# Kernel tuning notes

Measured on AMD Instinct MI355X. Metric: run time of the kernel, lower is better.

## Reference

```python
import jax, jax.numpy as jnp
import numpy as np

H_DIM = 2048
D_FF = 4 * H_DIM
NUM_EXPERTS = 8
NUM_SHARED = 2
BATCH, SEQ = 2, 2048


def setup_inputs() -> dict:
    key = jax.random.key(0)
    ks = jax.random.split(key, 10)
    s = 0.02
    return {
        "x": jax.random.normal(ks[0], (BATCH, SEQ, H_DIM), dtype=jnp.float32),
        "ws_w1": jax.random.normal(ks[1], (NUM_SHARED, H_DIM, D_FF), dtype=jnp.float32) * s,
        "ws_b1": jnp.zeros((NUM_SHARED, D_FF), dtype=jnp.float32),
        "ws_w2": jax.random.normal(ks[2], (NUM_SHARED, D_FF, H_DIM), dtype=jnp.float32) * s,
        "ws_b2": jnp.zeros((NUM_SHARED, H_DIM), dtype=jnp.float32),
        "we_w1": jax.random.normal(ks[3], (NUM_EXPERTS, H_DIM, D_FF), dtype=jnp.float32) * s,
        "we_b1": jnp.zeros((NUM_EXPERTS, D_FF), dtype=jnp.float32),
        "we_w2": jax.random.normal(ks[4], (NUM_EXPERTS, D_FF, H_DIM), dtype=jnp.float32) * s,
        "we_b2": jnp.zeros((NUM_EXPERTS, H_DIM), dtype=jnp.float32),
        "wg": jax.random.normal(ks[5], (H_DIM, NUM_EXPERTS), dtype=jnp.float32) * s,
        "top_k": 2,
    }


def reference(x, ws_w1, ws_b1, ws_w2, ws_b2, we_w1, we_b1, we_w2, we_b2, wg, top_k):
    B, S, D = x.shape
    xt = x.reshape(-1, D)  # [T, D], T = B*S
    T = xt.shape[0]

    # ---- shared experts: sum over NUM_SHARED dense MLPs ----
    hs = jax.nn.relu(jnp.einsum('td,ndf->ntf', xt, ws_w1) + ws_b1[:, None, :])
    shared = jnp.einsum('ntf,nfd->td', hs, ws_w2) + ws_b2.sum(axis=0)  # [T, D]

    # ---- sparse top-k routed MoE ----
    logits = xt @ wg                       # [T, E] router logits
    probs = jax.nn.softmax(logits, axis=-1)
    topv, topi = jax.lax.top_k(probs, top_k)
    gates = jnp.zeros_like(probs).at[jnp.arange(T)[:, None], topi].set(topv)  # [T, E]

    moe = jnp.zeros_like(xt)
    for e in range(we_w1.shape[0]):  # small fixed expert count
        he = jax.nn.relu(xt @ we_w1[e] + we_b1[e])
        ye = he @ we_w2[e] + we_b2[e]
        moe = moe + gates[:, e:e + 1] * ye

    out = (shared + moe).reshape(B, S, D)
    return out, logits
```

## Files before the change

kernel.cpp:

```cpp
#include <hip/hip_runtime.h>

#define TOKENS 4096
#define HD 2048
#define FF 8192
#define NE 8
#define NS 2

typedef __attribute__((ext_vector_type(8))) short bf16x8;
typedef __attribute__((ext_vector_type(4))) float f32x4;

__device__ __forceinline__ unsigned rnd_bf(unsigned u) {
  return u + 0x7fffu + ((u >> 16) & 1u);
}
__device__ __forceinline__ unsigned short f2bf(float f) {
  unsigned u = __builtin_bit_cast(unsigned, f);
  return (unsigned short)(rnd_bf(u) >> 16);
}

#define GLDS16(gp, lp)                                                         \
  __builtin_amdgcn_global_load_lds(                                            \
      (const __attribute__((address_space(1))) unsigned*)(const void*)(gp),    \
      (__attribute__((address_space(3))) unsigned*)(lp), 16, 0, 0)

__global__ void cast_x_kernel(const float* __restrict__ x, unsigned short* __restrict__ xb) {
  const size_t i = ((size_t)blockIdx.x * 256 + threadIdx.x) * 4;
  float4 v = *(const float4*)(x + i);
  ushort4 o;
  o.x = f2bf(v.x); o.y = f2bf(v.y); o.z = f2bf(v.z); o.w = f2bf(v.w);
  *(ushort4*)(xb + i) = o;
}

__global__ void router_kernel(const float* __restrict__ x, const float* __restrict__ wg,
                              float* __restrict__ logits_out, int* __restrict__ topi,
                              float* __restrict__ topv, int* __restrict__ counts) {
  const int wave = threadIdx.x >> 6, lane = threadIdx.x & 63;
  const int t = blockIdx.x * 4 + wave;
  const float* xr = x + (size_t)t * HD;
  float acc[8];
#pragma unroll
  for (int e = 0; e < 8; ++e) acc[e] = 0.f;
  for (int d = lane; d < HD; d += 64) {
    const float xv = xr[d];
    const float4 w0 = *(const float4*)(wg + (size_t)d * 8);
    const float4 w1 = *(const float4*)(wg + (size_t)d * 8 + 4);
    acc[0] += xv * w0.x; acc[1] += xv * w0.y; acc[2] += xv * w0.z; acc[3] += xv * w0.w;
    acc[4] += xv * w1.x; acc[5] += xv * w1.y; acc[6] += xv * w1.z; acc[7] += xv * w1.w;
  }
#pragma unroll
  for (int e = 0; e < 8; ++e) {
#pragma unroll
    for (int off = 32; off > 0; off >>= 1) acc[e] += __shfl_xor(acc[e], off);
  }
  if (lane == 0) {
    *(float4*)(logits_out + (size_t)t * 8)     = make_float4(acc[0], acc[1], acc[2], acc[3]);
    *(float4*)(logits_out + (size_t)t * 8 + 4) = make_float4(acc[4], acc[5], acc[6], acc[7]);
    float mx = acc[0];
#pragma unroll
    for (int e = 1; e < 8; ++e) mx = fmaxf(mx, acc[e]);
    float p[8], s = 0.f;
#pragma unroll
    for (int e = 0; e < 8; ++e) { p[e] = expf(acc[e] - mx); s += p[e]; }
    const float inv = 1.f / s;
    int i1 = 0;
#pragma unroll
    for (int e = 1; e < 8; ++e) if (acc[e] > acc[i1]) i1 = e;
    int i2 = (i1 == 0) ? 1 : 0;
#pragma unroll
    for (int e = 0; e < 8; ++e) if (e != i1 && acc[e] > acc[i2]) i2 = e;
    topi[2 * t]     = i1; topv[2 * t]     = p[i1] * inv;
    topi[2 * t + 1] = i2; topv[2 * t + 1] = p[i2] * inv;
    atomicAdd(&counts[i1], 1);
    atomicAdd(&counts[i2], 1);
  }
}

__global__ void offs_kernel(const int* __restrict__ counts, int* __restrict__ offs,
                            int* __restrict__ cursors) {
  if (threadIdx.x == 0) {
    int r = 0;
    for (int e = 0; e < NE; ++e) { offs[e] = r; cursors[e] = r; r += counts[e]; }
  }
}

__global__ void gather_kernel(const unsigned short* __restrict__ xb,
                              const int* __restrict__ topi, const float* __restrict__ topv,
                              int* __restrict__ cursors, unsigned short* __restrict__ xg,
                              int* __restrict__ row_token, float* __restrict__ row_gate) {
  const int wave = threadIdx.x >> 6, lane = threadIdx.x & 63;
  const int t = blockIdx.x * 4 + wave;
  const uint4* src = (const uint4*)(xb + (size_t)t * HD);
#pragma unroll
  for (int j = 0; j < 2; ++j) {
    const int e = topi[2 * t + j];
    int pos = 0;
    if (lane == 0) {
      pos = atomicAdd(&cursors[e], 1);
      row_token[pos] = t;
      row_gate[pos] = topv[2 * t + j];
    }
    pos = __shfl(pos, 0);
    uint4* dst = (uint4*)(xg + (size_t)pos * HD);
#pragma unroll
    for (int c = lane; c < 256; c += 64) dst[c] = src[c];
  }
}

template <int K, int N>
__global__ __launch_bounds__(256) void pack_wt(const float* __restrict__ we,
                                               const float* __restrict__ ws,
                                               unsigned short* __restrict__ dstw) {
  const int e = blockIdx.z;
  const float* src = (e < NE) ? (we + (size_t)e * K * N) : (ws + (size_t)(e - NE) * K * N);
  unsigned short* dst = dstw + (size_t)e * K * N;
  const int nt = blockIdx.x * 64;
  const int kt = blockIdx.y * 64;
  __shared__ unsigned short t[64][73];
  const int tid = threadIdx.x;
  const int rr = tid >> 4, cc = (tid & 15) * 4;
#pragma unroll
  for (int i = 0; i < 4; ++i) {
    const int k = rr + i * 16;
    float4 v = *(const float4*)(src + (size_t)(kt + k) * N + nt + cc);
    t[k][cc + 0] = f2bf(v.x);
    t[k][cc + 1] = f2bf(v.y);
    t[k][cc + 2] = f2bf(v.z);
    t[k][cc + 3] = f2bf(v.w);
  }
  __syncthreads();
  const int nr = tid >> 2, kc = (tid & 3) * 16;
  unsigned u[8];
#pragma unroll
  for (int j = 0; j < 8; ++j)
    u[j] = (unsigned)t[kc + 2 * j][nr] | ((unsigned)t[kc + 2 * j + 1][nr] << 16);
  unsigned short* dp = dst + (size_t)(nt + nr) * K + kt + kc;
  uint4 v0; v0.x = u[0]; v0.y = u[1]; v0.z = u[2]; v0.w = u[3];
  uint4 v1; v1.x = u[4]; v1.y = u[5]; v1.z = u[6]; v1.w = u[7];
  *(uint4*)dp = v0;
  *(uint4*)(dp + 8) = v1;
}

template <int MS>
__device__ __forceinline__ void rd_a(bf16x8 (&d)[8], const unsigned short* base,
                                     int wr, int fr, int fq, int swz) {
#pragma unroll
  for (int mi = 0; mi < 4; ++mi)
#pragma unroll
    for (int ks = 0; ks < 2; ++ks)
      d[mi * 2 + ks] = *(const bf16x8*)(base + (wr * 128 + MS * 64 + mi * 16 + fr) * 64 +
                                        (((ks * 4 + fq) ^ swz) << 3));
}
template <int NSUB>
__device__ __forceinline__ void rd_b(bf16x8 (&d)[4], const unsigned short* base,
                                     int wc, int fr, int fq, int swz) {
#pragma unroll
  for (int ni = 0; ni < 2; ++ni)
#pragma unroll
    for (int ks = 0; ks < 2; ++ks)
      d[ni * 2 + ks] = *(const bf16x8*)(base + (wc * 64 + NSUB * 32 + ni * 16 + fr) * 64 +
                                        (((ks * 4 + fq) ^ swz) << 3));
}
template <int MS, int NSUB>
__device__ __forceinline__ void mm16(f32x4 (&acc)[8][4], const bf16x8 (&a)[8],
                                     const bf16x8 (&b)[4]) {
  __builtin_amdgcn_s_setprio(1);
#pragma unroll
  for (int mi = 0; mi < 4; ++mi)
#pragma unroll
    for (int ni = 0; ni < 2; ++ni)
#pragma unroll
      for (int ks = 0; ks < 2; ++ks)
        acc[MS * 4 + mi][NSUB * 2 + ni] = __builtin_amdgcn_mfma_f32_16x16x32_bf16(
            a[mi * 2 + ks], b[ni * 2 + ks], acc[MS * 4 + mi][NSUB * 2 + ni], 0, 0, 0);
  __builtin_amdgcn_s_setprio(0);
}
template <int MS>
__device__ __forceinline__ void mm32(f32x4 (&acc)[8][4], const bf16x8 (&a)[8],
                                     const bf16x8 (&b0)[4], const bf16x8 (&b1)[4]) {
  __builtin_amdgcn_s_setprio(1);
#pragma unroll
  for (int mi = 0; mi < 4; ++mi)
#pragma unroll
    for (int nn = 0; nn < 4; ++nn)
#pragma unroll
      for (int ks = 0; ks < 2; ++ks) {
        const bf16x8& bb = (nn < 2) ? b0[(nn & 1) * 2 + ks] : b1[(nn & 1) * 2 + ks];
        acc[MS * 4 + mi][nn] = __builtin_amdgcn_mfma_f32_16x16x32_bf16(
            a[mi * 2 + ks], bb, acc[MS * 4 + mi][nn], 0, 0, 0);
      }
  __builtin_amdgcn_s_setprio(0);
}

#define PH_BAR_PRE()                                                           \
  __builtin_amdgcn_sched_barrier(0);                                           \
  __builtin_amdgcn_s_barrier();                                                \
  asm volatile("s_waitcnt lgkmcnt(0)" ::: "memory");                           \
  __builtin_amdgcn_sched_barrier(0)
#define PH_BAR_POST()                                                          \
  __builtin_amdgcn_sched_barrier(0);                                           \
  __builtin_amdgcn_s_barrier()

__global__ __launch_bounds__(512, 2) void gemm2p(
    const unsigned short* __restrict__ Ash,
    const unsigned short* __restrict__ Art,
    const unsigned short* __restrict__ wt,
    const float* __restrict__ bE, const float* __restrict__ bS,
    unsigned short* __restrict__ hout,
    const int* __restrict__ counts, const int* __restrict__ offs) {
  constexpr int K = HD;
  constexpr int NBX = FF / 256;
  constexpr int NWG = NBX * 16;
  extern __shared__ unsigned short smem[];

  const int e = blockIdx.z;
  int M;
  const unsigned short* A;
  const float* bias;
  int hbase;
  if (e < NE) {
    M = counts[e];
    A = Art + (size_t)offs[e] * K;
    bias = bE + (size_t)e * FF;
    hbase = offs[e];
  } else {
    M = TOKENS;
    A = Ash;
    bias = bS + (size_t)(e - NE) * FF;
    hbase = 2 * TOKENS + (e - NE) * TOKENS;
  }
  const unsigned short* Bt = wt + (size_t)e * HD * FF;

  int flat = blockIdx.x + NBX * blockIdx.y;
  flat = (flat & 7) * (NWG >> 3) + (flat >> 3);
  const int m0 = (flat & 15) * 256;
  const int n0 = (flat >> 4) * 256;
  if (m0 >= M) return;

  const int tid = threadIdx.x;
  const int wid = tid >> 6, ln = tid & 63;
  const int wr = wid >> 2, wc = wid & 3;
  const int fr = ln & 15, fq = ln >> 4;
  const int swz = fr & 7;

  const int lr8 = ln >> 3;
  const int lc8 = ln & 7;
  const int scol = (lc8 ^ lr8) << 3;
  const int wrA = wr * 128 + wc * 16;
  const int wcB = wc * 64 + wr * 16;

#define SA(s, kt, b)                                                           \
  { const int r0_ = wrA + (s) * 64 + lr8;                                      \
    const unsigned short* s_ = A + (size_t)(m0 + r0_) * K + (kt) * 64 + scol;  \
    unsigned short* d_ = smem + (b) * 32768 + r0_ * 64 + lc8 * 8;              \
    GLDS16(s_, d_); GLDS16(s_ + (size_t)8 * K, d_ + 8 * 64); }
#define SB(s, kt, b)                                                           \
  { const int r0_ = wcB + (s) * 32 + lr8;                                      \
    const unsigned short* s_ = Bt + (size_t)(n0 + r0_) * K + (kt) * 64 + scol; \
    unsigned short* d_ = smem + (b) * 32768 + 16384 + r0_ * 64 + lc8 * 8;      \
    GLDS16(s_, d_); GLDS16(s_ + (size_t)8 * K, d_ + 8 * 64); }

  f32x4 acc[8][4];
#pragma unroll
  for (int i = 0; i < 8; ++i)
#pragma unroll
    for (int j = 0; j < 4; ++j) acc[i][j] = (f32x4){0.f, 0.f, 0.f, 0.f};

  SA(0, 0, 0); SA(1, 0, 0); SB(0, 0, 0); SB(1, 0, 0);
  SA(0, 1, 1); SA(1, 1, 1); SB(0, 1, 1); SB(1, 1, 1);
  asm volatile("s_waitcnt vmcnt(8)" ::: "memory");
  __builtin_amdgcn_s_barrier();

  bf16x8 a0[8], a1[8], b0[4], b1[4];
  const int nkt = K / 64;
  for (int t = 0; t < nkt; ++t) {
    const int cur = t & 1;
    const int tp2 = (t + 2 < nkt) ? t + 2 : t;
    const unsigned short* As_c = smem + cur * 32768;
    const unsigned short* Bs_c = As_c + 16384;
    rd_a<0>(a0, As_c, wr, fr, fq, swz);
    rd_b<0>(b0, Bs_c, wc, fr, fq, swz);
    rd_b<1>(b1, Bs_c, wc, fr, fq, swz);
    asm volatile("s_waitcnt lgkmcnt(8)" ::: "memory");
    PH_BAR_PRE();
    mm32<0>(acc, a0, b0, b1);
    PH_BAR_POST();
    rd_a<1>(a1, As_c, wr, fr, fq, swz);
    SB(0, tp2, cur); SB(1, tp2, cur);
    PH_BAR_PRE();
    mm32<1>(acc, a1, b1, b0);
    __builtin_amdgcn_sched_barrier(0);
    SA(0, tp2, cur); SA(1, tp2, cur);
    __builtin_amdgcn_sched_barrier(0);
    asm volatile("s_waitcnt vmcnt(8)" ::: "memory");
    __builtin_amdgcn_s_barrier();
  }
#undef SA
#undef SB

#pragma unroll
  for (int nn = 0; nn < 4; ++nn) {
#pragma unroll
    for (int mm = 0; mm < 8; ++mm) {
      const int nsub_lo = (mm < 4) ? (nn >> 1) : 1 - (nn >> 1);
      const int col = n0 + wc * 64 + nsub_lo * 32 + (nn & 1) * 16 + fr;
      const float bb = bias[col];
#pragma unroll
      for (int j = 0; j < 4; ++j) {
        const int r = m0 + wr * 128 + (mm >> 2) * 64 + (mm & 3) * 16 + fq * 4 + j;
        if (r < M) {
          float v = acc[mm][nn][j] + bb;
          v = v > 0.f ? v : 0.f;
          hout[(size_t)(hbase + r) * FF + col] = f2bf(v);
        }
      }
    }
  }
}

__global__ __launch_bounds__(512, 2) void gemm8p(
    const unsigned short* __restrict__ hbuf,
    const unsigned short* __restrict__ wt,
    const float* __restrict__ bE, const float* __restrict__ bS,
    float* __restrict__ out,
    const int* __restrict__ counts, const int* __restrict__ offs,
    const int* __restrict__ row_token, const float* __restrict__ row_gate) {
  constexpr int K = FF;
  constexpr int NBX = HD / 256;
  constexpr int NWG = NBX * 16;
  extern __shared__ unsigned short smem[];

  const int e = blockIdx.z;
  const bool merged = (e == NE);
  int M;
  const unsigned short *A, *A2;
  const unsigned short *B, *B2;
  const float *bias, *bias2;
  const int* tok = nullptr;
  const float* gt = nullptr;

  if (!merged) {
    M = counts[e];
    const int off = offs[e];
    A = hbuf + (size_t)off * K;  A2 = A;
    tok = row_token + off; gt = row_gate + off;
    B = wt + (size_t)e * HD * FF;  B2 = B;
    bias = bE + (size_t)e * HD;  bias2 = bias;
  } else {
    M = TOKENS;
    A  = hbuf + (size_t)(2 * TOKENS) * K;
    A2 = hbuf + (size_t)(3 * TOKENS) * K;
    B  = wt + (size_t)NE * HD * FF;
    B2 = wt + (size_t)(NE + 1) * HD * FF;
    bias = bS;  bias2 = bS + HD;
  }

  int flat = blockIdx.x + NBX * blockIdx.y;
  flat = (flat & 7) * (NWG >> 3) + (flat >> 3);
  const int m0 = (flat & 15) * 256;
  const int n0 = (flat >> 4) * 256;
  if (m0 >= M) return;

  const int tid = threadIdx.x;
  const int wid = tid >> 6, ln = tid & 63;
  const int wr = wid >> 2, wc = wid & 3;
  const int fr = ln & 15, fq = ln >> 4;
  const int swz = fr & 7;

  const int lr8 = ln >> 3;
  const int lc8 = ln & 7;
  const int scol = (lc8 ^ lr8) << 3;
  const int wrA = wr * 128 + wc * 16;
  const int wcB = wc * 64 + wr * 16;

#define SA(s, kt, b)                                                           \
  { int kl_ = (kt); const unsigned short* ab_ = A;                             \
    if (merged && kl_ >= 128) { ab_ = A2; kl_ -= 128; }                        \
    const int r0_ = wrA + (s) * 64 + lr8;                                      \
    const unsigned short* s_ = ab_ + (size_t)(m0 + r0_) * K + kl_ * 64 + scol; \
    unsigned short* d_ = smem + (b) * 32768 + r0_ * 64 + lc8 * 8;              \
    GLDS16(s_, d_); GLDS16(s_ + (size_t)8 * K, d_ + 8 * 64); }
#define SB(s, kt, b)                                                           \
  { int kl_ = (kt); const unsigned short* bb_ = B;                             \
    if (merged && kl_ >= 128) { bb_ = B2; kl_ -= 128; }                        \
    const int r0_ = wcB + (s) * 32 + lr8;                                      \
    const unsigned short* s_ = bb_ + (size_t)(n0 + r0_) * K + kl_ * 64 + scol; \
    unsigned short* d_ = smem + (b) * 32768 + 16384 + r0_ * 64 + lc8 * 8;      \
    GLDS16(s_, d_); GLDS16(s_ + (size_t)8 * K, d_ + 8 * 64); }

  f32x4 acc[8][4];
#pragma unroll
  for (int i = 0; i < 8; ++i)
#pragma unroll
    for (int j = 0; j < 4; ++j) acc[i][j] = (f32x4){0.f, 0.f, 0.f, 0.f};

  SA(0, 0, 0); SA(1, 0, 0); SB(0, 0, 0); SB(1, 0, 0);
  SA(0, 1, 1); SA(1, 1, 1); SB(0, 1, 1); SB(1, 1, 1);
  asm volatile("s_waitcnt vmcnt(8)" ::: "memory");
  __builtin_amdgcn_s_barrier();

  bf16x8 a0[8], a1[8], b0[4], b1[4];
  const int nkt = merged ? 256 : 128;
  for (int t = 0; t < nkt; ++t) {
    const int cur = t & 1;
    const int tp2 = (t + 2 < nkt) ? t + 2 : t;
    const unsigned short* As_c = smem + cur * 32768;
    const unsigned short* Bs_c = As_c + 16384;
    rd_a<0>(a0, As_c, wr, fr, fq, swz);
    rd_b<0>(b0, Bs_c, wc, fr, fq, swz);
    asm volatile("s_waitcnt lgkmcnt(8)" ::: "memory");
    PH_BAR_PRE();
    mm16<0, 0>(acc, a0, b0);
    PH_BAR_POST();
    rd_b<1>(b1, Bs_c, wc, fr, fq, swz);
    SA(0, tp2, cur); SB(0, tp2, cur);
    PH_BAR_PRE();
    mm16<0, 1>(acc, a0, b1);
    PH_BAR_POST();
    rd_a<1>(a1, As_c, wr, fr, fq, swz);
    SB(1, tp2, cur);
    PH_BAR_PRE();
    mm16<1, 1>(acc, a1, b1);
    PH_BAR_POST();
    SA(1, tp2, cur);
    __builtin_amdgcn_sched_barrier(0);
    __builtin_amdgcn_s_barrier();
    __builtin_amdgcn_sched_barrier(0);
    mm16<1, 0>(acc, a1, b0);
    __builtin_amdgcn_sched_barrier(0);
    asm volatile("s_waitcnt vmcnt(8)" ::: "memory");
    __builtin_amdgcn_s_barrier();
  }
#undef SA
#undef SB

#pragma unroll
  for (int mm = 0; mm < 8; ++mm) {
#pragma unroll
    for (int j = 0; j < 4; ++j) {
      const int r = m0 + wr * 128 + (mm >> 2) * 64 + (mm & 3) * 16 + fq * 4 + j;
      if (r < M) {
        const int t = tok ? tok[r] : r;
        const float g = gt ? gt[r] : 1.f;
        float* orow = out + (size_t)t * HD + n0;
#pragma unroll
        for (int nn = 0; nn < 4; ++nn) {
          const int col = wc * 64 + (nn >> 1) * 32 + (nn & 1) * 16 + fr;
          float bb = bias[n0 + col];
          if (merged) bb += bias2[n0 + col];
          atomicAdd(orow + col, g * (acc[mm][nn][j] + bb));
        }
      }
    }
  }
}

extern "C" void kernel_launch(void* const* d_in, const int* in_sizes, int n_in,
                              void* d_out, int out_size, void* d_ws, size_t ws_size,
                              hipStream_t stream) {
  const float* x     = (const float*)d_in[0];
  const float* ws_w1 = (const float*)d_in[1];
  const float* ws_b1 = (const float*)d_in[2];
  const float* ws_w2 = (const float*)d_in[3];
  const float* ws_b2 = (const float*)d_in[4];
  const float* we_w1 = (const float*)d_in[5];
  const float* we_b1 = (const float*)d_in[6];
  const float* we_w2 = (const float*)d_in[7];
  const float* we_b2 = (const float*)d_in[8];
  const float* wg    = (const float*)d_in[9];

  float* out = (float*)d_out;
  float* logits = out + (size_t)TOKENS * HD;

  char* ws = (char*)d_ws;
  unsigned short* wt   = (unsigned short*)ws;
  unsigned short* xb   = (unsigned short*)(ws + 335544320);
  unsigned short* xg   = (unsigned short*)(ws + 352321536);
  unsigned short* hbuf = (unsigned short*)(ws + 386400256);
  char* ctrl = ws + 654835712;
  int*   row_token = (int*)(ctrl);
  float* row_gate  = (float*)(ctrl + 32768);
  int*   topi      = (int*)(ctrl + 65536);
  float* topv      = (float*)(ctrl + 98304);
  int*   counts    = (int*)(ctrl + 131072);
  int*   offs      = (int*)(ctrl + 131104);
  int*   cursors   = (int*)(ctrl + 131136);

  hipFuncSetAttribute(reinterpret_cast<const void*>(gemm2p),
                      hipFuncAttributeMaxDynamicSharedMemorySize, 131072);
  hipFuncSetAttribute(reinterpret_cast<const void*>(gemm8p),
                      hipFuncAttributeMaxDynamicSharedMemorySize, 131072);

  hipMemsetAsync(out, 0, (size_t)TOKENS * HD * sizeof(float), stream);
  hipMemsetAsync(counts, 0, NE * sizeof(int), stream);

  cast_x_kernel<<<8192, 256, 0, stream>>>(x, xb);
  router_kernel<<<1024, 256, 0, stream>>>(x, wg, logits, topi, topv, counts);
  offs_kernel<<<1, 64, 0, stream>>>(counts, offs, cursors);
  gather_kernel<<<1024, 256, 0, stream>>>(xb, topi, topv, cursors, xg, row_token, row_gate);

  pack_wt<HD, FF><<<dim3(FF / 64, HD / 64, 10), 256, 0, stream>>>(we_w1, ws_w1, wt);
  gemm2p<<<dim3(32, 16, 10), 512, 131072, stream>>>(
      xb, xg, wt, we_b1, ws_b1, hbuf, counts, offs);
  pack_wt<FF, HD><<<dim3(HD / 64, FF / 64, 10), 256, 0, stream>>>(we_w2, ws_w2, wt);
  gemm8p<<<dim3(8, 16, 9), 512, 131072, stream>>>(
      hbuf, wt, we_b2, ws_b2, out, counts, offs, row_token, row_gate);

  (void)in_sizes; (void)n_in; (void)out_size; (void)ws_size;
}
```

Before: 2.076 ms.

## Overlap W2 packing with first GEMM idle blocks and replace atomics with reduce

When the workspace is large enough, the W2 fp32-to-bf16 transpose/pack runs inside the first GEMM kernel, using the workgroups that would otherwise exit early because the routed experts have fewer rows. The second GEMM writes per-row fp32 outputs into a buffer instead of doing atomicAdd into the output. A separate reduce kernel then combines the shared and gated expert rows per token through a new row_of map. This removes the standalone pack kernel, the output memset and the atomics. In exchange it needs a larger workspace and an extra fp32 buffer write and read, and the old path is kept as a fallback.

```diff
diff --git a/kernel.cpp b/kernel.cpp
--- a/kernel.cpp
+++ b/kernel.cpp
@@ -85,7 +85,8 @@
 __global__ void gather_kernel(const unsigned short* __restrict__ xb,
                               const int* __restrict__ topi, const float* __restrict__ topv,
                               int* __restrict__ cursors, unsigned short* __restrict__ xg,
-                              int* __restrict__ row_token, float* __restrict__ row_gate) {
+                              int* __restrict__ row_token, float* __restrict__ row_gate,
+                              int* __restrict__ row_of) {
   const int wave = threadIdx.x >> 6, lane = threadIdx.x & 63;
   const int t = blockIdx.x * 4 + wave;
   const uint4* src = (const uint4*)(xb + (size_t)t * HD);
@@ -97,6 +98,7 @@
       pos = atomicAdd(&cursors[e], 1);
       row_token[pos] = t;
       row_gate[pos] = topv[2 * t + j];
+      row_of[2 * t + j] = pos;
     }
     pos = __shfl(pos, 0);
     uint4* dst = (uint4*)(xg + (size_t)pos * HD);
@@ -199,13 +201,14 @@
   __builtin_amdgcn_sched_barrier(0);                                           \
   __builtin_amdgcn_s_barrier()
 
-__global__ __launch_bounds__(512, 2) void gemm2p(
-    const unsigned short* __restrict__ Ash,
-    const unsigned short* __restrict__ Art,
-    const unsigned short* __restrict__ wt,
+__global__ __launch_bounds__(512, 2) void g1k(
+    const unsigned short* __restrict__ Ash, const unsigned short* __restrict__ Art,
+    const unsigned short* __restrict__ wt1,
     const float* __restrict__ bE, const float* __restrict__ bS,
     unsigned short* __restrict__ hout,
-    const int* __restrict__ counts, const int* __restrict__ offs) {
+    const int* __restrict__ counts, const int* __restrict__ offs,
+    int do_pack, const float* __restrict__ we_w2, const float* __restrict__ ws_w2,
+    unsigned short* __restrict__ wt2) {
   constexpr int K = HD;
   constexpr int NBX = FF / 256;
   constexpr int NWG = NBX * 16;
@@ -227,32 +230,77 @@
     bias = bS + (size_t)(e - NE) * FF;
     hbase = 2 * TOKENS + (e - NE) * TOKENS;
   }
-  const unsigned short* Bt = wt + (size_t)e * HD * FF;
+  const unsigned short* Bt = wt1 + (size_t)e * HD * FF;
 
   int flat = blockIdx.x + NBX * blockIdx.y;
   flat = (flat & 7) * (NWG >> 3) + (flat >> 3);
   const int m0 = (flat & 15) * 256;
   const int n0 = (flat >> 4) * 256;
-  if (m0 >= M) return;
-
   const int tid = threadIdx.x;
+
+  if (m0 >= M) {
+    if (!do_pack) return;
+    int total = 0, prefix = 0;
+    for (int e2 = 0; e2 < NE; ++e2) {
+      int mb = (counts[e2] + 255) >> 8; if (mb > 16) mb = 16;
+      const int inv = 32 * (16 - mb);
+      if (e2 < e) prefix += inv;
+      total += inv;
+    }
+    int mb_e = (counts[e] + 255) >> 8; if (mb_e > 16) mb_e = 16;
+    const int m_idx = flat & 15, n_idx = flat >> 4;
+    const int rank = prefix + n_idx * (16 - mb_e) + (m_idx - mb_e);
+    unsigned short* ps = smem;
+    const int NT = 10 * 128 * 32;
+    for (int i = rank; i < NT; i += total) {
+      const int e2 = i >> 12;
+      const int rem = i & 4095;
+      const int ktt = rem >> 5;
+      const int ntt = rem & 31;
+      const float* src = (e2 < NE) ? (we_w2 + (size_t)e2 * FF * HD)
+                                   : (ws_w2 + (size_t)(e2 - NE) * FF * HD);
+      unsigned short* dst = wt2 + (size_t)e2 * HD * FF;
+      __syncthreads();
+      {
+        const int kk = tid >> 3, cc = (tid & 7) * 8;
+        const float* sp = src + (size_t)(ktt * 64 + kk) * HD + ntt * 64 + cc;
+        const float4 v0 = *(const float4*)sp;
+        const float4 v1 = *(const float4*)(sp + 4);
+        unsigned short* tp = ps + kk * 72 + cc;
+        tp[0] = f2bf(v0.x); tp[1] = f2bf(v0.y); tp[2] = f2bf(v0.z); tp[3] = f2bf(v0.w);
+        tp[4] = f2bf(v1.x); tp[5] = f2bf(v1.y); tp[6] = f2bf(v1.z); tp[7] = f2bf(v1.w);
+      }
+      __syncthreads();
+      {
+        const int nn = tid >> 3, kc = (tid & 7) * 8;
+        unsigned u[4];
+#pragma unroll
+        for (int j = 0; j < 4; ++j)
+          u[j] = (unsigned)ps[(kc + 2 * j) * 72 + nn] |
+                 ((unsigned)ps[(kc + 2 * j + 1) * 72 + nn] << 16);
+        uint4 v; v.x = u[0]; v.y = u[1]; v.z = u[2]; v.w = u[3];
+        *(uint4*)(dst + (size_t)(ntt * 64 + nn) * FF + ktt * 64 + kc) = v;
+      }
+    }
+    return;
+  }
+
   const int wid = tid >> 6, ln = tid & 63;
   const int wr = wid >> 2, wc = wid & 3;
   const int fr = ln & 15, fq = ln >> 4;
   const int swz = fr & 7;
-
   const int lr8 = ln >> 3;
   const int lc8 = ln & 7;
   const int scol = (lc8 ^ lr8) << 3;
   const int wrA = wr * 128 + wc * 16;
   const int wcB = wc * 64 + wr * 16;
 
-#define SA(s, kt, b)                                                           \
+#define SA1(s, kt, b)                                                          \
   { const int r0_ = wrA + (s) * 64 + lr8;                                      \
     const unsigned short* s_ = A + (size_t)(m0 + r0_) * K + (kt) * 64 + scol;  \
     unsigned short* d_ = smem + (b) * 32768 + r0_ * 64 + lc8 * 8;              \
     GLDS16(s_, d_); GLDS16(s_ + (size_t)8 * K, d_ + 8 * 64); }
-#define SB(s, kt, b)                                                           \
+#define SB1(s, kt, b)                                                          \
   { const int r0_ = wcB + (s) * 32 + lr8;                                      \
     const unsigned short* s_ = Bt + (size_t)(n0 + r0_) * K + (kt) * 64 + scol; \
     unsigned short* d_ = smem + (b) * 32768 + 16384 + r0_ * 64 + lc8 * 8;      \
@@ -264,8 +312,8 @@
 #pragma unroll
     for (int j = 0; j < 4; ++j) acc[i][j] = (f32x4){0.f, 0.f, 0.f, 0.f};
 
-  SA(0, 0, 0); SA(1, 0, 0); SB(0, 0, 0); SB(1, 0, 0);
-  SA(0, 1, 1); SA(1, 1, 1); SB(0, 1, 1); SB(1, 1, 1);
+  SA1(0, 0, 0); SA1(1, 0, 0); SB1(0, 0, 0); SB1(1, 0, 0);
+  SA1(0, 1, 1); SA1(1, 1, 1); SB1(0, 1, 1); SB1(1, 1, 1);
   asm volatile("s_waitcnt vmcnt(8)" ::: "memory");
   __builtin_amdgcn_s_barrier();
 
@@ -284,17 +332,17 @@
     mm32<0>(acc, a0, b0, b1);
     PH_BAR_POST();
     rd_a<1>(a1, As_c, wr, fr, fq, swz);
-    SB(0, tp2, cur); SB(1, tp2, cur);
+    SB1(0, tp2, cur); SB1(1, tp2, cur);
     PH_BAR_PRE();
     mm32<1>(acc, a1, b1, b0);
     __builtin_amdgcn_sched_barrier(0);
-    SA(0, tp2, cur); SA(1, tp2, cur);
+    SA1(0, tp2, cur); SA1(1, tp2, cur);
     __builtin_amdgcn_sched_barrier(0);
     asm volatile("s_waitcnt vmcnt(8)" ::: "memory");
     __builtin_amdgcn_s_barrier();
   }
-#undef SA
-#undef SB
+#undef SA1
+#undef SB1
 
 #pragma unroll
   for (int nn = 0; nn < 4; ++nn) {
@@ -313,6 +361,143 @@
         }
       }
     }
+  }
+}
+
+__global__ __launch_bounds__(512, 2) void g2k(
+    const unsigned short* __restrict__ hbuf, const unsigned short* __restrict__ wt2,
+    const float* __restrict__ bE, const float* __restrict__ bS,
+    float* __restrict__ ybuf,
+    const int* __restrict__ counts, const int* __restrict__ offs) {
+  constexpr int K = FF;
+  constexpr int NBX = HD / 256;
+  constexpr int NWG = NBX * 16;
+  extern __shared__ unsigned short smem[];
+
+  const int e = blockIdx.z;
+  int M;
+  const unsigned short* A;
+  const float* bias;
+  int hbase;
+  if (e < NE) {
+    M = counts[e];
+    A = hbuf + (size_t)offs[e] * K;
+    bias = bE + (size_t)e * HD;
+    hbase = offs[e];
+  } else {
+    M = TOKENS;
+    hbase = 2 * TOKENS + (e - NE) * TOKENS;
+    A = hbuf + (size_t)hbase * K;
+    bias = bS + (size_t)(e - NE) * HD;
+  }
+  const unsigned short* Bt = wt2 + (size_t)e * HD * FF;
+
+  int flat = blockIdx.x + NBX * blockIdx.y;
+  flat = (flat & 7) * (NWG >> 3) + (flat >> 3);
+  const int m0 = (flat & 15) * 256;
+  const int n0 = (flat >> 4) * 256;
+  if (m0 >= M) return;
+
+  const int tid = threadIdx.x;
+  const int wid = tid >> 6, ln = tid & 63;
+  const int wr = wid >> 2, wc = wid & 3;
+  const int fr = ln & 15, fq = ln >> 4;
+  const int swz = fr & 7;
+  const int lr8 = ln >> 3;
+  const int lc8 = ln & 7;
+  const int scol = (lc8 ^ lr8) << 3;
+  const int wrA = wr * 128 + wc * 16;
+  const int wcB = wc * 64 + wr * 16;
+
+#define SA2(s, kt, b)                                                          \
+  { const int r0_ = wrA + (s) * 64 + lr8;                                      \
+    const unsigned short* s_ = A + (size_t)(m0 + r0_) * K + (kt) * 64 + scol;  \
+    unsigned short* d_ = smem + (b) * 32768 + r0_ * 64 + lc8 * 8;              \
+    GLDS16(s_, d_); GLDS16(s_ + (size_t)8 * K, d_ + 8 * 64); }
+#define SB2(s, kt, b)                                                          \
+  { const int r0_ = wcB + (s) * 32 + lr8;                                      \
+    const unsigned short* s_ = Bt + (size_t)(n0 + r0_) * K + (kt) * 64 + scol; \
+    unsigned short* d_ = smem + (b) * 32768 + 16384 + r0_ * 64 + lc8 * 8;      \
+    GLDS16(s_, d_); GLDS16(s_ + (size_t)8 * K, d_ + 8 * 64); }
+
+  f32x4 acc[8][4];
+#pragma unroll
+  for (int i = 0; i < 8; ++i)
+#pragma unroll
+    for (int j = 0; j < 4; ++j) acc[i][j] = (f32x4){0.f, 0.f, 0.f, 0.f};
+
+  SA2(0, 0, 0); SA2(1, 0, 0); SB2(0, 0, 0); SB2(1, 0, 0);
+  SA2(0, 1, 1); SA2(1, 1, 1); SB2(0, 1, 1); SB2(1, 1, 1);
+  asm volatile("s_waitcnt vmcnt(8)" ::: "memory");
+  __builtin_amdgcn_s_barrier();
+
+  bf16x8 a0[8], a1[8], b0[4], b1[4];
+  const int nkt = K / 64;
+  for (int t = 0; t < nkt; ++t) {
+    const int cur = t & 1;
+    const int tp2 = (t + 2 < nkt) ? t + 2 : t;
+    const unsigned short* As_c = smem + cur * 32768;
+    const unsigned short* Bs_c = As_c + 16384;
+    rd_a<0>(a0, As_c, wr, fr, fq, swz);
+    rd_b<0>(b0, Bs_c, wc, fr, fq, swz);
+    rd_b<1>(b1, Bs_c, wc, fr, fq, swz);
+    asm volatile("s_waitcnt lgkmcnt(8)" ::: "memory");
+    PH_BAR_PRE();
+    mm32<0>(acc, a0, b0, b1);
+    PH_BAR_POST();
+    rd_a<1>(a1, As_c, wr, fr, fq, swz);
+    SB2(0, tp2, cur); SB2(1, tp2, cur);
+    PH_BAR_PRE();
+    mm32<1>(acc, a1, b1, b0);
+    __builtin_amdgcn_sched_barrier(0);
+    SA2(0, tp2, cur); SA2(1, tp2, cur);
+    __builtin_amdgcn_sched_barrier(0);
+    asm volatile("s_waitcnt vmcnt(8)" ::: "memory");
+    __builtin_amdgcn_s_barrier();
+  }
+#undef SA2
+#undef SB2
+
+#pragma unroll
+  for (int nn = 0; nn < 4; ++nn) {
+#pragma unroll
+    for (int mm = 0; mm < 8; ++mm) {
+      const int nsub_lo = (mm < 4) ? (nn >> 1) : 1 - (nn >> 1);
+      const int colw = wc * 64 + nsub_lo * 32 + (nn & 1) * 16 + fr;
+      const float bb = bias[n0 + colw];
+#pragma unroll
+      for (int j = 0; j < 4; ++j) {
+        const int r = m0 + wr * 128 + (mm >> 2) * 64 + (mm & 3) * 16 + fq * 4 + j;
+        if (r < M)
+          ybuf[(size_t)(hbase + r) * HD + n0 + colw] = acc[mm][nn][j] + bb;
+      }
+    }
+  }
+}
+
+__global__ __launch_bounds__(256) void reduce_kernel(
+    const float* __restrict__ ybuf, const int* __restrict__ row_of,
+    const float* __restrict__ topv, float* __restrict__ out) {
+  const int t = blockIdx.x;
+  const int d = threadIdx.x * 8;
+  const float g0 = topv[2 * t], g1 = topv[2 * t + 1];
+  const float* y0 = ybuf + (size_t)row_of[2 * t] * HD + d;
+  const float* y1 = ybuf + (size_t)row_of[2 * t + 1] * HD + d;
+  const float* s0 = ybuf + (size_t)(2 * TOKENS + t) * HD + d;
+  const float* s1 = ybuf + (size_t)(3 * TOKENS + t) * HD + d;
+  float* o = out + (size_t)t * HD + d;
+#pragma unroll
+  for (int q = 0; q < 2; ++q) {
+    const float4 a = *(const float4*)(s0 + q * 4);
+    const float4 b = *(const float4*)(s1 + q * 4);
+    const float4 c = *(const float4*)(y0 + q * 4);
+    const float4 e = *(const float4*)(y1 + q * 4);
+    float4 r;
+    r.x = a.x + b.x + g0 * c.x + g1 * e.x;
+    r.y = a.y + b.y + g0 * c.y + g1 * e.y;
+    r.z = a.z + b.z + g0 * c.z + g1 * e.z;
+    r.w = a.w + b.w + g0 * c.w + g1 * e.w;
+    *(float4*)(o + q * 4) = r;
   }
 }
 
@@ -364,21 +549,20 @@
   const int wr = wid >> 2, wc = wid & 3;
   const int fr = ln & 15, fq = ln >> 4;
   const int swz = fr & 7;
-
   const int lr8 = ln >> 3;
   const int lc8 = ln & 7;
   const int scol = (lc8 ^ lr8) << 3;
   const int wrA = wr * 128 + wc * 16;
   const int wcB = wc * 64 + wr * 16;
 
-#define SA(s, kt, b)                                                           \
+#define SAF(s, kt, b)                                                          \
   { int kl_ = (kt); const unsigned short* ab_ = A;                             \
     if (merged && kl_ >= 128) { ab_ = A2; kl_ -= 128; }                        \
     const int r0_ = wrA + (s) * 64 + lr8;                                      \
     const unsigned short* s_ = ab_ + (size_t)(m0 + r0_) * K + kl_ * 64 + scol; \
     unsigned short* d_ = smem + (b) * 32768 + r0_ * 64 + lc8 * 8;              \
     GLDS16(s_, d_); GLDS16(s_ + (size_t)8 * K, d_ + 8 * 64); }
-#define SB(s, kt, b)                                                           \
+#define SBF(s, kt, b)                                                          \
   { int kl_ = (kt); const unsigned short* bb_ = B;                             \
     if (merged && kl_ >= 128) { bb_ = B2; kl_ -= 128; }                        \
     const int r0_ = wcB + (s) * 32 + lr8;                                      \
@@ -392,8 +576,8 @@
 #pragma unroll
     for (int j = 0; j < 4; ++j) acc[i][j] = (f32x4){0.f, 0.f, 0.f, 0.f};
 
-  SA(0, 0, 0); SA(1, 0, 0); SB(0, 0, 0); SB(1, 0, 0);
-  SA(0, 1, 1); SA(1, 1, 1); SB(0, 1, 1); SB(1, 1, 1);
+  SAF(0, 0, 0); SAF(1, 0, 0); SBF(0, 0, 0); SBF(1, 0, 0);
+  SAF(0, 1, 1); SAF(1, 1, 1); SBF(0, 1, 1); SBF(1, 1, 1);
   asm volatile("s_waitcnt vmcnt(8)" ::: "memory");
   __builtin_amdgcn_s_barrier();
 
@@ -411,16 +595,16 @@
     mm16<0, 0>(acc, a0, b0);
     PH_BAR_POST();
     rd_b<1>(b1, Bs_c, wc, fr, fq, swz);
-    SA(0, tp2, cur); SB(0, tp2, cur);
+    SAF(0, tp2, cur); SBF(0, tp2, cur);
     PH_BAR_PRE();
     mm16<0, 1>(acc, a0, b1);
     PH_BAR_POST();
     rd_a<1>(a1, As_c, wr, fr, fq, swz);
-    SB(1, tp2, cur);
+    SBF(1, tp2, cur);
     PH_BAR_PRE();
     mm16<1, 1>(acc, a1, b1);
     PH_BAR_POST();
-    SA(1, tp2, cur);
+    SAF(1, tp2, cur);
     __builtin_amdgcn_sched_barrier(0);
     __builtin_amdgcn_s_barrier();
     __builtin_amdgcn_sched_barrier(0);
@@ -429,8 +613,8 @@
     asm volatile("s_waitcnt vmcnt(8)" ::: "memory");
     __builtin_amdgcn_s_barrier();
   }
-#undef SA
-#undef SB
+#undef SAF
+#undef SBF
 
 #pragma unroll
   for (int mm = 0; mm < 8; ++mm) {
@@ -470,39 +654,76 @@
   float* out = (float*)d_out;
   float* logits = out + (size_t)TOKENS * HD;
 
-  char* ws = (char*)d_ws;
-  unsigned short* wt   = (unsigned short*)ws;
-  unsigned short* xb   = (unsigned short*)(ws + 335544320);
-  unsigned short* xg   = (unsigned short*)(ws + 352321536);
-  unsigned short* hbuf = (unsigned short*)(ws + 386400256);
-  char* ctrl = ws + 654835712;
-  int*   row_token = (int*)(ctrl);
-  float* row_gate  = (float*)(ctrl + 32768);
-  int*   topi      = (int*)(ctrl + 65536);
-  float* topv      = (float*)(ctrl + 98304);
-  int*   counts    = (int*)(ctrl + 131072);
-  int*   offs      = (int*)(ctrl + 131104);
-  int*   cursors   = (int*)(ctrl + 131136);
-
-  hipFuncSetAttribute(reinterpret_cast<const void*>(gemm2p),
+  hipFuncSetAttribute(reinterpret_cast<const void*>(g1k),
+                      hipFuncAttributeMaxDynamicSharedMemorySize, 131072);
+  hipFuncSetAttribute(reinterpret_cast<const void*>(g2k),
                       hipFuncAttributeMaxDynamicSharedMemorySize, 131072);
   hipFuncSetAttribute(reinterpret_cast<const void*>(gemm8p),
                       hipFuncAttributeMaxDynamicSharedMemorySize, 131072);
 
-  hipMemsetAsync(out, 0, (size_t)TOKENS * HD * sizeof(float), stream);
-  hipMemsetAsync(counts, 0, NE * sizeof(int), stream);
-
-  cast_x_kernel<<<8192, 256, 0, stream>>>(x, xb);
-  router_kernel<<<1024, 256, 0, stream>>>(x, wg, logits, topi, topv, counts);
-  offs_kernel<<<1, 64, 0, stream>>>(counts, offs, cursors);
-  gather_kernel<<<1024, 256, 0, stream>>>(xb, topi, topv, cursors, xg, row_token, row_gate);
-
-  pack_wt<HD, FF><<<dim3(FF / 64, HD / 64, 10), 256, 0, stream>>>(we_w1, ws_w1, wt);
-  gemm2p<<<dim3(32, 16, 10), 512, 131072, stream>>>(
-      xb, xg, wt, we_b1, ws_b1, hbuf, counts, offs);
-  pack_wt<FF, HD><<<dim3(HD / 64, FF / 64, 10), 256, 0, stream>>>(we_w2, ws_w2, wt);
-  gemm8p<<<dim3(8, 16, 9), 512, 131072, stream>>>(
-      hbuf, wt, we_b2, ws_b2, out, counts, offs, row_token, row_gate);
+  const size_t NEED2 = 990544000ull;
+  char* ws = (char*)d_ws;
+
+  if (ws_size >= NEED2) {
+    unsigned short* wt1  = (unsigned short*)ws;
+    unsigned short* wt2  = (unsigned short*)(ws + 335544320);
+    unsigned short* xb   = (unsigned short*)(ws + 671088640);
+    unsigned short* xg   = (unsigned short*)(ws + 687865856);
+    unsigned short* hbuf = (unsigned short*)(ws + 721944576);
+    char* ctrl = ws + 990380032;
+    float* ybuf = (float*)ws;
+    int*   row_token = (int*)(ctrl);
+    float* row_gate  = (float*)(ctrl + 32768);
+    int*   topi      = (int*)(ctrl + 65536);
+    float* topv      = (float*)(ctrl + 98304);
+    int*   counts    = (int*)(ctrl + 131072);
+    int*   offs      = (int*)(ctrl + 131104);
+    int*   cursors   = (int*)(ctrl + 131136);
+    int*   row_of    = (int*)(ctrl + 131168);
+
+    hipMemsetAsync(counts, 0, NE * sizeof(int), stream);
+    cast_x_kernel<<<8192, 256, 0, stream>>>(x, xb);
+    router_kernel<<<1024, 256, 0, stream>>>(x, wg, logits, topi, topv, counts);
+    offs_kernel<<<1, 64, 0, stream>>>(counts, offs, cursors);
+    gather_kernel<<<1024, 256, 0, stream>>>(xb, topi, topv, cursors, xg,
+                                            row_token, row_gate, row_of);
+    pack_wt<HD, FF><<<dim3(FF / 64, HD / 64, 10), 256, 0, stream>>>(we_w1, ws_w1, wt1);
+    g1k<<<dim3(32, 16, 10), 512, 131072, stream>>>(
+        xb, xg, wt1, we_b1, ws_b1, hbuf, counts, offs, 1, we_w2, ws_w2, wt2);
+    g2k<<<dim3(8, 16, 10), 512, 131072, stream>>>(
+        hbuf, wt2, we_b2, ws_b2, ybuf, counts, offs);
+    reduce_kernel<<<TOKENS, 256, 0, stream>>>(ybuf, row_of, topv, out);
+  } else {
+    unsigned short* wt   = (unsigned short*)ws;
+    unsigned short* xb   = (unsigned short*)(ws + 335544320);
+    unsigned short* xg   = (unsigned short*)(ws + 352321536);
+    unsigned short* hbuf = (unsigned short*)(ws + 386400256);
+    char* ctrl = ws + 654835712;
+    int*   row_token = (int*)(ctrl);
+    float* row_gate  = (float*)(ctrl + 32768);
+    int*   topi      = (int*)(ctrl + 65536);
+    float* topv      = (float*)(ctrl + 98304);
+    int*   counts    = (int*)(ctrl + 131072);
+    int*   offs      = (int*)(ctrl + 131104);
+    int*   cursors   = (int*)(ctrl + 131136);
+    int*   row_of    = (int*)(ctrl + 131168);
+
+    hipMemsetAsync(out, 0, (size_t)TOKENS * HD * sizeof(float), stream);
+    hipMemsetAsync(counts, 0, NE * sizeof(int), stream);
+
+    cast_x_kernel<<<8192, 256, 0, stream>>>(x, xb);
+    router_kernel<<<1024, 256, 0, stream>>>(x, wg, logits, topi, topv, counts);
+    offs_kernel<<<1, 64, 0, stream>>>(counts, offs, cursors);
+    gather_kernel<<<1024, 256, 0, stream>>>(xb, topi, topv, cursors, xg,
+                                            row_token, row_gate, row_of);
+
+    pack_wt<HD, FF><<<dim3(FF / 64, HD / 64, 10), 256, 0, stream>>>(we_w1, ws_w1, wt);
+    g1k<<<dim3(32, 16, 10), 512, 131072, stream>>>(
+        xb, xg, wt, we_b1, ws_b1, hbuf, counts, offs, 0, nullptr, nullptr, nullptr);
+    pack_wt<FF, HD><<<dim3(HD / 64, FF / 64, 10), 256, 0, stream>>>(we_w2, ws_w2, wt);
+    gemm8p<<<dim3(8, 16, 9), 512, 131072, stream>>>(
+        hbuf, wt, we_b2, ws_b2, out, counts, offs, row_token, row_gate);
+  }
 
   (void)in_sizes; (void)n_in; (void)out_size; (void)ws_size;
 }
```

After: 2.033 ms. -2.1%, faster.
